# Kernel tuning notes

Hardware: AMD Instinct MI355X
Metric: run time of the kernel (lower is better)

The kernel has to match this reference:

```python
import jax, jax.numpy as jnp
import numpy as np

NEG = -1e9

def setup_inputs() -> dict:
    key = jax.random.key(0)
    k1, k2, k3, k4 = jax.random.split(key, 4)
    L, B, D = 4096, 4, 64
    query = jax.random.normal(k1, (L, B, D), dtype=jnp.float32)
    kkey = jax.random.normal(k2, (L, B, D), dtype=jnp.float32)
    value = jax.random.normal(k3, (L, B, D), dtype=jnp.float32)
    key_padding_mask = jax.random.randint(k4, (B, L), 0, 2).astype(jnp.bool_)
    return {"query": query, "key": kkey, "value": value, "key_padding_mask": key_padding_mask}

def reference(query, key, value, key_padding_mask):
    # [L, B, D] -> [B, L, D]
    scaling = float(query.shape[-1]) ** (-0.5)
    q = jnp.transpose(query, (1, 0, 2)) * scaling
    k = jnp.transpose(key, (1, 0, 2))
    v = jnp.transpose(value, (1, 0, 2))
    attn = jnp.einsum('bqd,bkd->bqk', q, k)  # [B, Lq, Lk]
    attn = jnp.where(key_padding_mask[:, None, :], NEG, attn)
    attn = jax.nn.softmax(attn, axis=-1)  # dropout p=0 -> identity
    out = jnp.einsum('bqk,bkd->bqd', attn, v)
    return jnp.transpose(out, (1, 0, 2)), attn
```

## Files before the change

kernel.cpp:

```cpp
#include <hip/hip_runtime.h>
#include <math.h>

#define L_ 4096
#define B_ 4
#define D_ 64
#define JS 8

typedef float f32x4 __attribute__((ext_vector_type(4)));
typedef int   i32x4 __attribute__((ext_vector_type(4)));
typedef short bf16x8 __attribute__((ext_vector_type(8)));
typedef unsigned short u16x8 __attribute__((ext_vector_type(8)));
typedef unsigned short u16x4 __attribute__((ext_vector_type(4)));

#define MFMA16(a, b, c) __builtin_amdgcn_mfma_f32_16x16x32_bf16(a, b, c, 0, 0, 0)

__device__ inline unsigned short f2bf(float x) {
    union { float f; unsigned int u; } v; v.f = x;
    unsigned int r = v.u + 0x7FFFu + ((v.u >> 16) & 1u);
    return (unsigned short)(r >> 16);
}
__device__ inline float bf2f(unsigned short h) {
    union { unsigned int u; float f; } v; v.u = ((unsigned int)h) << 16;
    return v.f;
}

__device__ inline void stage64(const unsigned short* __restrict__ g,
                               unsigned short* l, int tid) {
    const int w  = tid >> 6;
    const int ln = tid & 63;
#pragma unroll
    for (int r2 = 0; r2 < 2; ++r2) {
        const int base = r2 * 4096 + w * 1024;
        const int d = base + ln * 16;
        const int s = d ^ (((d >> 7) & 7) << 4);
        __builtin_amdgcn_global_load_lds(
            (const __attribute__((address_space(1))) void*)((const char*)g + s),
            (__attribute__((address_space(3))) void*)((char*)l + base),
            16, 0, 0);
    }
}

__device__ inline bf16x8 rdfrag(const unsigned short* l, int row, int colh) {
    int off = (row << 7) + (colh << 1);
    off ^= (row & 7) << 4;
    return *(const bf16x8*)((const char*)l + off);
}

__global__ void zero_out_kernel(float* __restrict__ out) {
    const int i = blockIdx.x * 256 + threadIdx.x;
    ((f32x4*)out)[i] = (f32x4){0.f, 0.f, 0.f, 0.f};
}

__device__ inline void convert16(const float* __restrict__ src,
                                 unsigned short* __restrict__ dhi,
                                 unsigned short* __restrict__ dlo) {
    f32x4 a[4];
#pragma unroll
    for (int i = 0; i < 4; ++i) a[i] = *(const f32x4*)(src + 4 * i);
    u16x8 h0, h1, lo0, lo1;
#pragma unroll
    for (int m = 0; m < 16; ++m) {
        float x = a[m >> 2][m & 3];
        unsigned short h = f2bf(x);
        unsigned short l = f2bf(x - bf2f(h));
        if (m < 8) { h0[m] = (short)h; lo0[m] = (short)l; }
        else       { h1[m - 8] = (short)h; lo1[m - 8] = (short)l; }
    }
    *(u16x8*)(dhi)     = h0;  *(u16x8*)(dhi + 8) = h1;
    *(u16x8*)(dlo)     = lo0; *(u16x8*)(dlo + 8) = lo1;
}

__global__ __launch_bounds__(256) void prep_kernel(
    const float* __restrict__ Q, const float* __restrict__ K, const float* __restrict__ V,
    unsigned short* __restrict__ Qhi, unsigned short* __restrict__ Qlo,
    unsigned short* __restrict__ Khi, unsigned short* __restrict__ Klo,
    unsigned short* __restrict__ Vthi, unsigned short* __restrict__ Vtlo) {
    __shared__ __align__(16) float vt[64][68];
    const int t  = threadIdx.x;
    const int b  = blockIdx.x >> 6;
    const int l0 = (blockIdx.x & 63) << 6;
    const int r  = t >> 2;
    const int d0 = (t & 3) << 4;

    const size_t src = (size_t)(l0 + r) * (B_ * D_) + (size_t)b * D_ + d0;
    const size_t dst = ((size_t)b * L_ + l0 + r) * D_ + d0;
    convert16(Q + src, Qhi + dst, Qlo + dst);
    convert16(K + src, Khi + dst, Klo + dst);

    const float* vsrc = V + src;
#pragma unroll
    for (int m = 0; m < 16; m += 4)
        *(f32x4*)&vt[r][d0 + m] = *(const f32x4*)&vsrc[m];
    __syncthreads();

    const int d  = t >> 2;
    const int lp = (t & 3) << 4;
    u16x8 h0, h1, lo0, lo1;
#pragma unroll
    for (int m = 0; m < 16; ++m) {
        float x = vt[lp + m][d];
        unsigned short h = f2bf(x);
        unsigned short l = f2bf(x - bf2f(h));
        if (m < 8) { h0[m] = (short)h; lo0[m] = (short)l; }
        else       { h1[m - 8] = (short)h; lo1[m - 8] = (short)l; }
    }
    unsigned short* oh = Vthi + ((size_t)b * D_ + d) * L_ + l0 + lp;
    unsigned short* ol = Vtlo + ((size_t)b * D_ + d) * L_ + l0 + lp;
    *(u16x8*)(oh) = h0;  *(u16x8*)(oh + 8) = h1;
    *(u16x8*)(ol) = lo0; *(u16x8*)(ol + 8) = lo1;
}

__global__ __launch_bounds__(256) void stats_kernel(
    const unsigned short* __restrict__ Qhi, const unsigned short* __restrict__ Qlo,
    const unsigned short* __restrict__ Khi, const unsigned short* __restrict__ Klo,
    const int* __restrict__ mask, float* __restrict__ lpart)
{
    __shared__ __align__(16) unsigned short kh[2][64 * 64];
    __shared__ __align__(16) unsigned short kl[2][64 * 64];

    const int tid = threadIdx.x;
    const int w = tid >> 6, lane = tid & 63;
    const int lr = lane & 15, lg = lane >> 4;
    const int b  = blockIdx.x >> 8;
    const int it = (blockIdx.x >> 3) & 31;
    const int jc = blockIdx.x & 7;
    const int irow = it * 128 + w * 32;
    const int j0c  = jc * (L_ / JS);

    bf16x8 qh0[2], qh1[2], ql0[2], ql1[2];
#pragma unroll
    for (int rs = 0; rs < 2; ++rs) {
        const size_t qoff = ((size_t)b * L_ + irow + rs * 16 + lr) * D_ + lg * 8;
        qh0[rs] = *(const bf16x8*)(Qhi + qoff);
        qh1[rs] = *(const bf16x8*)(Qhi + qoff + 32);
        ql0[rs] = *(const bf16x8*)(Qlo + qoff);
        ql1[rs] = *(const bf16x8*)(Qlo + qoff + 32);
    }

    float lsum[2] = {0.f, 0.f};
    int buf = 0;
    stage64(Khi + ((size_t)b * L_ + j0c) * D_, kh[0], tid);
    stage64(Klo + ((size_t)b * L_ + j0c) * D_, kl[0], tid);
    __syncthreads();

    for (int st = 0; st < (L_ / JS) / 64; ++st) {
        const int j0 = j0c + st * 64;
        if (st < (L_ / JS) / 64 - 1) {
            stage64(Khi + ((size_t)b * L_ + j0 + 64) * D_, kh[buf ^ 1], tid);
            stage64(Klo + ((size_t)b * L_ + j0 + 64) * D_, kl[buf ^ 1], tid);
        }
#pragma unroll
        for (int jj = 0; jj < 4; ++jj) {
            const bf16x8 a_h0 = rdfrag(kh[buf], jj * 16 + lr, lg * 8);
            const bf16x8 a_h1 = rdfrag(kh[buf], jj * 16 + lr, lg * 8 + 32);
            const bf16x8 a_l0 = rdfrag(kl[buf], jj * 16 + lr, lg * 8);
            const bf16x8 a_l1 = rdfrag(kl[buf], jj * 16 + lr, lg * 8 + 32);
            const i32x4 mv = *(const i32x4*)&mask[(size_t)b * L_ + j0 + jj * 16 + lg * 4];
            f32x4 bias;
#pragma unroll
            for (int r = 0; r < 4; ++r) bias[r] = mv[r] ? -1.0e9f : 0.0f;
#pragma unroll
            for (int rs = 0; rs < 2; ++rs) {
                f32x4 acc = {0.f, 0.f, 0.f, 0.f};
                acc = MFMA16(a_h0, qh0[rs], acc);
                acc = MFMA16(a_h1, qh1[rs], acc);
                acc = MFMA16(a_h0, ql0[rs], acc);
                acc = MFMA16(a_h1, ql1[rs], acc);
                acc = MFMA16(a_l0, qh0[rs], acc);
                acc = MFMA16(a_l1, qh1[rs], acc);
#pragma unroll
                for (int r = 0; r < 4; ++r)
                    lsum[rs] += __expf(fmaf(acc[r], 0.125f, bias[r]) - 32.0f);
            }
        }
        __syncthreads();
        buf ^= 1;
    }
#pragma unroll
    for (int rs = 0; rs < 2; ++rs) {
        float v = lsum[rs];
        v += __shfl_xor(v, 16, 64);
        v += __shfl_xor(v, 32, 64);
        if (lg == 0)
            lpart[((size_t)b * L_ + irow + rs * 16 + lr) * JS + jc] = v;
    }
}

__global__ __launch_bounds__(256) void pv_kernel(
    const unsigned short* __restrict__ Qhi, const unsigned short* __restrict__ Qlo,
    const unsigned short* __restrict__ Khi, const unsigned short* __restrict__ Klo,
    const unsigned short* __restrict__ Vthi, const unsigned short* __restrict__ Vtlo,
    const int* __restrict__ mask, const float* __restrict__ lpart,
    float* __restrict__ attn, float* __restrict__ out)
{
    __shared__ __align__(16) unsigned short kh[2][64 * 64];
    __shared__ __align__(16) unsigned short kl[2][64 * 64];
    __shared__ __align__(16) unsigned short phs[4][16][72];
    __shared__ __align__(16) unsigned short pls[4][16][72];

    const int tid = threadIdx.x;
    const int w = tid >> 6, lane = tid & 63;
    const int lr = lane & 15, lg = lane >> 4;
    const int b  = blockIdx.x >> 8;
    const int it = (blockIdx.x >> 3) & 31;
    const int jc = blockIdx.x & 7;
    const int irow = it * 128 + w * 32;
    const int j0c  = jc * (L_ / JS);
    const size_t ab = (size_t)b * L_ * L_;

    bf16x8 qh0[2], qh1[2], ql0[2], ql1[2];
    float invl[2];
#pragma unroll
    for (int rs = 0; rs < 2; ++rs) {
        const size_t row = (size_t)b * L_ + irow + rs * 16 + lr;
        const size_t qoff = row * D_ + lg * 8;
        qh0[rs] = *(const bf16x8*)(Qhi + qoff);
        qh1[rs] = *(const bf16x8*)(Qhi + qoff + 32);
        ql0[rs] = *(const bf16x8*)(Qlo + qoff);
        ql1[rs] = *(const bf16x8*)(Qlo + qoff + 32);
        const float* lp = lpart + row * JS;
        f32x4 s0 = *(const f32x4*)lp;
        f32x4 s1 = *(const f32x4*)(lp + 4);
        invl[rs] = 1.0f / (s0[0] + s0[1] + s0[2] + s0[3] + s1[0] + s1[1] + s1[2] + s1[3]);
    }

    f32x4 oacc[2][4];
#pragma unroll
    for (int rs = 0; rs < 2; ++rs)
#pragma unroll
        for (int dv = 0; dv < 4; ++dv) oacc[rs][dv] = (f32x4){0.f, 0.f, 0.f, 0.f};

    int buf = 0;
    stage64(Khi + ((size_t)b * L_ + j0c) * D_, kh[0], tid);
    stage64(Klo + ((size_t)b * L_ + j0c) * D_, kl[0], tid);
    __syncthreads();

    for (int st = 0; st < (L_ / JS) / 64; ++st) {
        const int j0 = j0c + st * 64;
        if (st < (L_ / JS) / 64 - 1) {
            stage64(Khi + ((size_t)b * L_ + j0 + 64) * D_, kh[buf ^ 1], tid);
            stage64(Klo + ((size_t)b * L_ + j0 + 64) * D_, kl[buf ^ 1], tid);
        }
#pragma unroll
        for (int rs = 0; rs < 2; ++rs) {
#pragma unroll
            for (int jj = 0; jj < 4; ++jj) {
                const bf16x8 a_h0 = rdfrag(kh[buf], jj * 16 + lr, lg * 8);
                const bf16x8 a_h1 = rdfrag(kh[buf], jj * 16 + lr, lg * 8 + 32);
                const bf16x8 a_l0 = rdfrag(kl[buf], jj * 16 + lr, lg * 8);
                const bf16x8 a_l1 = rdfrag(kl[buf], jj * 16 + lr, lg * 8 + 32);
                const i32x4 mv = *(const i32x4*)&mask[(size_t)b * L_ + j0 + jj * 16 + lg * 4];
                f32x4 acc = {0.f, 0.f, 0.f, 0.f};
                acc = MFMA16(a_h0, qh0[rs], acc);
                acc = MFMA16(a_h1, qh1[rs], acc);
                acc = MFMA16(a_h0, ql0[rs], acc);
                acc = MFMA16(a_h1, ql1[rs], acc);
                acc = MFMA16(a_l0, qh0[rs], acc);
                acc = MFMA16(a_l1, qh1[rs], acc);
                f32x4 p4;
                u16x4 hv, lv;
#pragma unroll
                for (int r = 0; r < 4; ++r) {
                    const float bias = mv[r] ? -1.0e9f : 0.0f;
                    const float p = __expf(fmaf(acc[r], 0.125f, bias) - 32.0f) * invl[rs];
                    p4[r] = p;
                    const unsigned short h = f2bf(p);
                    hv[r] = h;
                    lv[r] = f2bf(p - bf2f(h));
                }
                *(f32x4*)&attn[ab + (size_t)(irow + rs * 16 + lr) * L_ + j0 + jj * 16 + lg * 4] = p4;
                *(u16x4*)&phs[w][lr][jj * 16 + lg * 4] = hv;
                *(u16x4*)&pls[w][lr][jj * 16 + lg * 4] = lv;
            }
#pragma unroll
            for (int kk = 0; kk < 2; ++kk) {
                const bf16x8 ph = *(const bf16x8*)&phs[w][lr][kk * 32 + lg * 8];
                const bf16x8 pl = *(const bf16x8*)&pls[w][lr][kk * 32 + lg * 8];
#pragma unroll
                for (int dv = 0; dv < 4; ++dv) {
                    const size_t voff = ((size_t)b * D_ + dv * 16 + lr) * L_ + j0 + kk * 32 + lg * 8;
                    const bf16x8 vh = *(const bf16x8*)(Vthi + voff);
                    const bf16x8 vl = *(const bf16x8*)(Vtlo + voff);
                    oacc[rs][dv] = MFMA16(vh, ph, oacc[rs][dv]);
                    oacc[rs][dv] = MFMA16(vh, pl, oacc[rs][dv]);
                    oacc[rs][dv] = MFMA16(vl, ph, oacc[rs][dv]);
                }
            }
        }
        __syncthreads();
        buf ^= 1;
    }

#pragma unroll
    for (int rs = 0; rs < 2; ++rs)
#pragma unroll
        for (int dv = 0; dv < 4; ++dv) {
            const size_t obase = (size_t)(irow + rs * 16 + lr) * (B_ * D_) + b * D_ + dv * 16 + lg * 4;
#pragma unroll
            for (int r = 0; r < 4; ++r)
                atomicAdd(&out[obase + r], oacc[rs][dv][r]);
        }
}

extern "C" void kernel_launch(void* const* d_in, const int* in_sizes, int n_in,
                              void* d_out, int out_size, void* d_ws, size_t ws_size,
                              hipStream_t stream) {
    const float* Q   = (const float*)d_in[0];
    const float* K   = (const float*)d_in[1];
    const float* V   = (const float*)d_in[2];
    const int*  mask = (const int*)d_in[3];

    float* out  = (float*)d_out;
    float* attn = (float*)d_out + (size_t)L_ * B_ * D_;

    const size_t NE = (size_t)B_ * L_ * D_;
    unsigned short* Qhi  = (unsigned short*)d_ws;
    unsigned short* Qlo  = Qhi + NE;
    unsigned short* Khi  = Qhi + 2 * NE;
    unsigned short* Klo  = Qhi + 3 * NE;
    unsigned short* Vthi = Qhi + 4 * NE;
    unsigned short* Vtlo = Qhi + 5 * NE;
    float* lpart = (float*)((char*)d_ws + 6 * NE * sizeof(unsigned short));

    hipLaunchKernelGGL(zero_out_kernel, dim3((L_ * B_ * D_) / (256 * 4)), dim3(256), 0, stream, out);
    hipLaunchKernelGGL(prep_kernel, dim3(B_ * (L_ / 64)), dim3(256), 0, stream,
                       Q, K, V, Qhi, Qlo, Khi, Klo, Vthi, Vtlo);
    hipLaunchKernelGGL(stats_kernel, dim3(B_ * (L_ / 128) * JS), dim3(256), 0, stream,
                       Qhi, Qlo, Khi, Klo, mask, lpart);
    hipLaunchKernelGGL(pv_kernel, dim3(B_ * (L_ / 128) * JS), dim3(256), 0, stream,
                       Qhi, Qlo, Khi, Klo, Vthi, Vtlo, mask, lpart, attn, out);
}
```

Measured before the change: 579.4 us.

## Fuse stats and PV passes into one kernel, normalize attention afterwards

Removes the separate softmax-denominator kernel, which recomputed the full QK^T product. One kernel now computes the unnormalized exponentials once, writes them to attn, feeds them to the PV MFMAs, and emits partial row sums. New rescale and finalize kernels then divide attn and out by the summed denominator. The 1/sqrt(D) scale is folded into Q during prep, and the exponent no longer subtracts a fixed offset. The trade-offs are an extra full read and write of the large attn matrix, and the loss of K-tile double buffering in the fused loop.

```diff
diff --git a/kernel.cpp b/kernel.cpp
--- a/kernel.cpp
+++ b/kernel.cpp
@@ -51,7 +51,7 @@
     ((f32x4*)out)[i] = (f32x4){0.f, 0.f, 0.f, 0.f};
 }
 
-__device__ inline void convert16(const float* __restrict__ src,
+__device__ inline void convert16(const float* __restrict__ src, float scale,
                                  unsigned short* __restrict__ dhi,
                                  unsigned short* __restrict__ dlo) {
     f32x4 a[4];
@@ -60,7 +60,7 @@
     u16x8 h0, h1, lo0, lo1;
 #pragma unroll
     for (int m = 0; m < 16; ++m) {
-        float x = a[m >> 2][m & 3];
+        float x = a[m >> 2][m & 3] * scale;
         unsigned short h = f2bf(x);
         unsigned short l = f2bf(x - bf2f(h));
         if (m < 8) { h0[m] = (short)h; lo0[m] = (short)l; }
@@ -84,8 +84,8 @@
 
     const size_t src = (size_t)(l0 + r) * (B_ * D_) + (size_t)b * D_ + d0;
     const size_t dst = ((size_t)b * L_ + l0 + r) * D_ + d0;
-    convert16(Q + src, Qhi + dst, Qlo + dst);
-    convert16(K + src, Khi + dst, Klo + dst);
+    convert16(Q + src, 0.125f, Qhi + dst, Qlo + dst);
+    convert16(K + src, 1.0f,   Khi + dst, Klo + dst);
 
     const float* vsrc = V + src;
 #pragma unroll
@@ -110,91 +110,15 @@
     *(u16x8*)(ol) = lo0; *(u16x8*)(ol + 8) = lo1;
 }
 
-__global__ __launch_bounds__(256) void stats_kernel(
-    const unsigned short* __restrict__ Qhi, const unsigned short* __restrict__ Qlo,
-    const unsigned short* __restrict__ Khi, const unsigned short* __restrict__ Klo,
-    const int* __restrict__ mask, float* __restrict__ lpart)
-{
-    __shared__ __align__(16) unsigned short kh[2][64 * 64];
-    __shared__ __align__(16) unsigned short kl[2][64 * 64];
-
-    const int tid = threadIdx.x;
-    const int w = tid >> 6, lane = tid & 63;
-    const int lr = lane & 15, lg = lane >> 4;
-    const int b  = blockIdx.x >> 8;
-    const int it = (blockIdx.x >> 3) & 31;
-    const int jc = blockIdx.x & 7;
-    const int irow = it * 128 + w * 32;
-    const int j0c  = jc * (L_ / JS);
-
-    bf16x8 qh0[2], qh1[2], ql0[2], ql1[2];
-#pragma unroll
-    for (int rs = 0; rs < 2; ++rs) {
-        const size_t qoff = ((size_t)b * L_ + irow + rs * 16 + lr) * D_ + lg * 8;
-        qh0[rs] = *(const bf16x8*)(Qhi + qoff);
-        qh1[rs] = *(const bf16x8*)(Qhi + qoff + 32);
-        ql0[rs] = *(const bf16x8*)(Qlo + qoff);
-        ql1[rs] = *(const bf16x8*)(Qlo + qoff + 32);
-    }
-
-    float lsum[2] = {0.f, 0.f};
-    int buf = 0;
-    stage64(Khi + ((size_t)b * L_ + j0c) * D_, kh[0], tid);
-    stage64(Klo + ((size_t)b * L_ + j0c) * D_, kl[0], tid);
-    __syncthreads();
-
-    for (int st = 0; st < (L_ / JS) / 64; ++st) {
-        const int j0 = j0c + st * 64;
-        if (st < (L_ / JS) / 64 - 1) {
-            stage64(Khi + ((size_t)b * L_ + j0 + 64) * D_, kh[buf ^ 1], tid);
-            stage64(Klo + ((size_t)b * L_ + j0 + 64) * D_, kl[buf ^ 1], tid);
-        }
-#pragma unroll
-        for (int jj = 0; jj < 4; ++jj) {
-            const bf16x8 a_h0 = rdfrag(kh[buf], jj * 16 + lr, lg * 8);
-            const bf16x8 a_h1 = rdfrag(kh[buf], jj * 16 + lr, lg * 8 + 32);
-            const bf16x8 a_l0 = rdfrag(kl[buf], jj * 16 + lr, lg * 8);
-            const bf16x8 a_l1 = rdfrag(kl[buf], jj * 16 + lr, lg * 8 + 32);
-            const i32x4 mv = *(const i32x4*)&mask[(size_t)b * L_ + j0 + jj * 16 + lg * 4];
-            f32x4 bias;
-#pragma unroll
-            for (int r = 0; r < 4; ++r) bias[r] = mv[r] ? -1.0e9f : 0.0f;
-#pragma unroll
-            for (int rs = 0; rs < 2; ++rs) {
-                f32x4 acc = {0.f, 0.f, 0.f, 0.f};
-                acc = MFMA16(a_h0, qh0[rs], acc);
-                acc = MFMA16(a_h1, qh1[rs], acc);
-                acc = MFMA16(a_h0, ql0[rs], acc);
-                acc = MFMA16(a_h1, ql1[rs], acc);
-                acc = MFMA16(a_l0, qh0[rs], acc);
-                acc = MFMA16(a_l1, qh1[rs], acc);
-#pragma unroll
-                for (int r = 0; r < 4; ++r)
-                    lsum[rs] += __expf(fmaf(acc[r], 0.125f, bias[r]) - 32.0f);
-            }
-        }
-        __syncthreads();
-        buf ^= 1;
-    }
-#pragma unroll
-    for (int rs = 0; rs < 2; ++rs) {
-        float v = lsum[rs];
-        v += __shfl_xor(v, 16, 64);
-        v += __shfl_xor(v, 32, 64);
-        if (lg == 0)
-            lpart[((size_t)b * L_ + irow + rs * 16 + lr) * JS + jc] = v;
-    }
-}
-
-__global__ __launch_bounds__(256) void pv_kernel(
+__global__ __launch_bounds__(256) void fused_kernel(
     const unsigned short* __restrict__ Qhi, const unsigned short* __restrict__ Qlo,
     const unsigned short* __restrict__ Khi, const unsigned short* __restrict__ Klo,
     const unsigned short* __restrict__ Vthi, const unsigned short* __restrict__ Vtlo,
-    const int* __restrict__ mask, const float* __restrict__ lpart,
-    float* __restrict__ attn, float* __restrict__ out)
+    const int* __restrict__ mask, float* __restrict__ attn,
+    float* __restrict__ lpart, float* __restrict__ out)
 {
-    __shared__ __align__(16) unsigned short kh[2][64 * 64];
-    __shared__ __align__(16) unsigned short kl[2][64 * 64];
+    __shared__ __align__(16) unsigned short kh[64 * 64];
+    __shared__ __align__(16) unsigned short kl[64 * 64];
     __shared__ __align__(16) unsigned short phs[4][16][72];
     __shared__ __align__(16) unsigned short pls[4][16][72];
 
@@ -209,19 +133,13 @@
     const size_t ab = (size_t)b * L_ * L_;
 
     bf16x8 qh0[2], qh1[2], ql0[2], ql1[2];
-    float invl[2];
 #pragma unroll
     for (int rs = 0; rs < 2; ++rs) {
-        const size_t row = (size_t)b * L_ + irow + rs * 16 + lr;
-        const size_t qoff = row * D_ + lg * 8;
+        const size_t qoff = ((size_t)b * L_ + irow + rs * 16 + lr) * D_ + lg * 8;
         qh0[rs] = *(const bf16x8*)(Qhi + qoff);
         qh1[rs] = *(const bf16x8*)(Qhi + qoff + 32);
         ql0[rs] = *(const bf16x8*)(Qlo + qoff);
         ql1[rs] = *(const bf16x8*)(Qlo + qoff + 32);
-        const float* lp = lpart + row * JS;
-        f32x4 s0 = *(const f32x4*)lp;
-        f32x4 s1 = *(const f32x4*)(lp + 4);
-        invl[rs] = 1.0f / (s0[0] + s0[1] + s0[2] + s0[3] + s1[0] + s1[1] + s1[2] + s1[3]);
     }
 
     f32x4 oacc[2][4];
@@ -229,27 +147,29 @@
     for (int rs = 0; rs < 2; ++rs)
 #pragma unroll
         for (int dv = 0; dv < 4; ++dv) oacc[rs][dv] = (f32x4){0.f, 0.f, 0.f, 0.f};
-
-    int buf = 0;
-    stage64(Khi + ((size_t)b * L_ + j0c) * D_, kh[0], tid);
-    stage64(Klo + ((size_t)b * L_ + j0c) * D_, kl[0], tid);
-    __syncthreads();
+    float lsum[2] = {0.f, 0.f};
 
     for (int st = 0; st < (L_ / JS) / 64; ++st) {
         const int j0 = j0c + st * 64;
-        if (st < (L_ / JS) / 64 - 1) {
-            stage64(Khi + ((size_t)b * L_ + j0 + 64) * D_, kh[buf ^ 1], tid);
-            stage64(Klo + ((size_t)b * L_ + j0 + 64) * D_, kl[buf ^ 1], tid);
-        }
+        __syncthreads();
+        stage64(Khi + ((size_t)b * L_ + j0) * D_, kh, tid);
+        stage64(Klo + ((size_t)b * L_ + j0) * D_, kl, tid);
+        __syncthreads();
+
+        i32x4 mv[4];
+#pragma unroll
+        for (int jj = 0; jj < 4; ++jj)
+            mv[jj] = *(const i32x4*)&mask[(size_t)b * L_ + j0 + jj * 16 + lg * 4];
+
+        bf16x8 P[2][4];
 #pragma unroll
         for (int rs = 0; rs < 2; ++rs) {
 #pragma unroll
             for (int jj = 0; jj < 4; ++jj) {
-                const bf16x8 a_h0 = rdfrag(kh[buf], jj * 16 + lr, lg * 8);
-                const bf16x8 a_h1 = rdfrag(kh[buf], jj * 16 + lr, lg * 8 + 32);
-                const bf16x8 a_l0 = rdfrag(kl[buf], jj * 16 + lr, lg * 8);
-                const bf16x8 a_l1 = rdfrag(kl[buf], jj * 16 + lr, lg * 8 + 32);
-                const i32x4 mv = *(const i32x4*)&mask[(size_t)b * L_ + j0 + jj * 16 + lg * 4];
+                const bf16x8 a_h0 = rdfrag(kh, jj * 16 + lr, lg * 8);
+                const bf16x8 a_h1 = rdfrag(kh, jj * 16 + lr, lg * 8 + 32);
+                const bf16x8 a_l0 = rdfrag(kl, jj * 16 + lr, lg * 8);
+                const bf16x8 a_l1 = rdfrag(kl, jj * 16 + lr, lg * 8 + 32);
                 f32x4 acc = {0.f, 0.f, 0.f, 0.f};
                 acc = MFMA16(a_h0, qh0[rs], acc);
                 acc = MFMA16(a_h1, qh1[rs], acc);
@@ -257,42 +177,51 @@
                 acc = MFMA16(a_h1, ql1[rs], acc);
                 acc = MFMA16(a_l0, qh0[rs], acc);
                 acc = MFMA16(a_l1, qh1[rs], acc);
-                f32x4 p4;
+                f32x4 e4;
                 u16x4 hv, lv;
 #pragma unroll
                 for (int r = 0; r < 4; ++r) {
-                    const float bias = mv[r] ? -1.0e9f : 0.0f;
-                    const float p = __expf(fmaf(acc[r], 0.125f, bias) - 32.0f) * invl[rs];
-                    p4[r] = p;
-                    const unsigned short h = f2bf(p);
+                    const float s = mv[jj][r] ? -1.0e9f : acc[r];
+                    const float e = __expf(s);
+                    e4[r] = e;
+                    const unsigned short h = f2bf(e);
                     hv[r] = h;
-                    lv[r] = f2bf(p - bf2f(h));
+                    lv[r] = f2bf(e - bf2f(h));
                 }
-                *(f32x4*)&attn[ab + (size_t)(irow + rs * 16 + lr) * L_ + j0 + jj * 16 + lg * 4] = p4;
+                lsum[rs] += e4[0] + e4[1] + e4[2] + e4[3];
+                *(f32x4*)&attn[ab + (size_t)(irow + rs * 16 + lr) * L_ + j0 + jj * 16 + lg * 4] = e4;
                 *(u16x4*)&phs[w][lr][jj * 16 + lg * 4] = hv;
                 *(u16x4*)&pls[w][lr][jj * 16 + lg * 4] = lv;
             }
-#pragma unroll
-            for (int kk = 0; kk < 2; ++kk) {
-                const bf16x8 ph = *(const bf16x8*)&phs[w][lr][kk * 32 + lg * 8];
-                const bf16x8 pl = *(const bf16x8*)&pls[w][lr][kk * 32 + lg * 8];
-#pragma unroll
-                for (int dv = 0; dv < 4; ++dv) {
-                    const size_t voff = ((size_t)b * D_ + dv * 16 + lr) * L_ + j0 + kk * 32 + lg * 8;
-                    const bf16x8 vh = *(const bf16x8*)(Vthi + voff);
-                    const bf16x8 vl = *(const bf16x8*)(Vtlo + voff);
-                    oacc[rs][dv] = MFMA16(vh, ph, oacc[rs][dv]);
-                    oacc[rs][dv] = MFMA16(vh, pl, oacc[rs][dv]);
-                    oacc[rs][dv] = MFMA16(vl, ph, oacc[rs][dv]);
+            P[rs][0] = *(const bf16x8*)&phs[w][lr][lg * 8];
+            P[rs][1] = *(const bf16x8*)&pls[w][lr][lg * 8];
+            P[rs][2] = *(const bf16x8*)&phs[w][lr][32 + lg * 8];
+            P[rs][3] = *(const bf16x8*)&pls[w][lr][32 + lg * 8];
+        }
+#pragma unroll
+        for (int kk = 0; kk < 2; ++kk) {
+#pragma unroll
+            for (int dv = 0; dv < 4; ++dv) {
+                const size_t voff = ((size_t)b * D_ + dv * 16 + lr) * L_ + j0 + kk * 32 + lg * 8;
+                const bf16x8 vh = *(const bf16x8*)(Vthi + voff);
+                const bf16x8 vl = *(const bf16x8*)(Vtlo + voff);
+#pragma unroll
+                for (int rs = 0; rs < 2; ++rs) {
+                    oacc[rs][dv] = MFMA16(vh, P[rs][kk * 2], oacc[rs][dv]);
+                    oacc[rs][dv] = MFMA16(vh, P[rs][kk * 2 + 1], oacc[rs][dv]);
+                    oacc[rs][dv] = MFMA16(vl, P[rs][kk * 2], oacc[rs][dv]);
                 }
             }
         }
-        __syncthreads();
-        buf ^= 1;
-    }
-
-#pragma unroll
-    for (int rs = 0; rs < 2; ++rs)
+    }
+
+#pragma unroll
+    for (int rs = 0; rs < 2; ++rs) {
+        float v = lsum[rs];
+        v += __shfl_xor(v, 16, 64);
+        v += __shfl_xor(v, 32, 64);
+        if (lg == 0)
+            lpart[((size_t)b * L_ + irow + rs * 16 + lr) * JS + jc] = v;
 #pragma unroll
         for (int dv = 0; dv < 4; ++dv) {
             const size_t obase = (size_t)(irow + rs * 16 + lr) * (B_ * D_) + b * D_ + dv * 16 + lg * 4;
@@ -300,6 +229,43 @@
             for (int r = 0; r < 4; ++r)
                 atomicAdd(&out[obase + r], oacc[rs][dv][r]);
         }
+    }
+}
+
+__global__ __launch_bounds__(256) void rescale_kernel(
+    float* __restrict__ attn, const float* __restrict__ lpart)
+{
+    const int row = blockIdx.x;
+    const float* lp = lpart + (size_t)row * JS;
+    float l = 0.f;
+#pragma unroll
+    for (int k = 0; k < JS; ++k) l += lp[k];
+    const float invl = 1.0f / l;
+
+    float* base = attn + (size_t)row * L_;
+    const int t = threadIdx.x;
+#pragma unroll
+    for (int k = 0; k < 4; ++k) {
+        f32x4 v = *(f32x4*)&base[(k * 256 + t) * 4];
+        v[0] *= invl; v[1] *= invl; v[2] *= invl; v[3] *= invl;
+        *(f32x4*)&base[(k * 256 + t) * 4] = v;
+    }
+}
+
+__global__ __launch_bounds__(256) void finalize_kernel(
+    float* __restrict__ out, const float* __restrict__ lpart)
+{
+    const int idx = blockIdx.x * 256 + threadIdx.x;
+    const int lb  = idx >> 4;
+    const int l   = lb >> 2, b = lb & 3;
+    const float* lp = lpart + ((size_t)b * L_ + l) * JS;
+    float s = 0.f;
+#pragma unroll
+    for (int k = 0; k < JS; ++k) s += lp[k];
+    const float invl = 1.0f / s;
+    f32x4 v = ((f32x4*)out)[idx];
+    v[0] *= invl; v[1] *= invl; v[2] *= invl; v[3] *= invl;
+    ((f32x4*)out)[idx] = v;
 }
 
 extern "C" void kernel_launch(void* const* d_in, const int* in_sizes, int n_in,
@@ -325,8 +291,9 @@
     hipLaunchKernelGGL(zero_out_kernel, dim3((L_ * B_ * D_) / (256 * 4)), dim3(256), 0, stream, out);
     hipLaunchKernelGGL(prep_kernel, dim3(B_ * (L_ / 64)), dim3(256), 0, stream,
                        Q, K, V, Qhi, Qlo, Khi, Klo, Vthi, Vtlo);
-    hipLaunchKernelGGL(stats_kernel, dim3(B_ * (L_ / 128) * JS), dim3(256), 0, stream,
-                       Qhi, Qlo, Khi, Klo, mask, lpart);
-    hipLaunchKernelGGL(pv_kernel, dim3(B_ * (L_ / 128) * JS), dim3(256), 0, stream,
-                       Qhi, Qlo, Khi, Klo, Vthi, Vtlo, mask, lpart, attn, out);
-}
+    hipLaunchKernelGGL(fused_kernel, dim3(B_ * (L_ / 128) * JS), dim3(256), 0, stream,
+                       Qhi, Qlo, Khi, Klo, Vthi, Vtlo, mask, attn, lpart, out);
+    hipLaunchKernelGGL(rescale_kernel, dim3(B_ * L_), dim3(256), 0, stream, attn, lpart);
+    hipLaunchKernelGGL(finalize_kernel, dim3((L_ * B_ * D_) / (256 * 4)), dim3(256), 0, stream,
+                       out, lpart);
+}
```

Result: faster. 525.6 us (-9.3%).

## Fold softmax scale into Q prep and reuse V fragments across row sets

Applied to the files above, without the earlier changes.

The 1/sqrt(D) scale moves into the Q bf16 split in the prep kernel, and the constant -32 shift is dropped from both exp passes. This removes an fma and a subtract per score element. In the PV kernel, V fragments and mask words are now loaded once per 64-key step and shared by both 16-row sets, where before they were reloaded inside the row-set loop. The P-times-V MFMAs are regrouped after both P tiles are built. The K tile is now single-buffered with two barriers per step, which gives up the prefetch overlap and raises register pressure. Dropping the shift also gives up its overflow headroom in exp.

```diff
diff --git a/kernel.cpp b/kernel.cpp
--- a/kernel.cpp
+++ b/kernel.cpp
@@ -5,6 +5,7 @@
 #define B_ 4
 #define D_ 64
 #define JS 8
+#define NS ((L_ / JS) / 64)
 
 typedef float f32x4 __attribute__((ext_vector_type(4)));
 typedef int   i32x4 __attribute__((ext_vector_type(4)));
@@ -51,7 +52,7 @@
     ((f32x4*)out)[i] = (f32x4){0.f, 0.f, 0.f, 0.f};
 }
 
-__device__ inline void convert16(const float* __restrict__ src,
+__device__ inline void convert16(const float* __restrict__ src, float scale,
                                  unsigned short* __restrict__ dhi,
                                  unsigned short* __restrict__ dlo) {
     f32x4 a[4];
@@ -60,7 +61,7 @@
     u16x8 h0, h1, lo0, lo1;
 #pragma unroll
     for (int m = 0; m < 16; ++m) {
-        float x = a[m >> 2][m & 3];
+        float x = a[m >> 2][m & 3] * scale;
         unsigned short h = f2bf(x);
         unsigned short l = f2bf(x - bf2f(h));
         if (m < 8) { h0[m] = (short)h; lo0[m] = (short)l; }
@@ -84,8 +85,8 @@
 
     const size_t src = (size_t)(l0 + r) * (B_ * D_) + (size_t)b * D_ + d0;
     const size_t dst = ((size_t)b * L_ + l0 + r) * D_ + d0;
-    convert16(Q + src, Qhi + dst, Qlo + dst);
-    convert16(K + src, Khi + dst, Klo + dst);
+    convert16(Q + src, 0.125f, Qhi + dst, Qlo + dst);
+    convert16(K + src, 1.0f,   Khi + dst, Klo + dst);
 
     const float* vsrc = V + src;
 #pragma unroll
@@ -143,9 +144,9 @@
     stage64(Klo + ((size_t)b * L_ + j0c) * D_, kl[0], tid);
     __syncthreads();
 
-    for (int st = 0; st < (L_ / JS) / 64; ++st) {
+    for (int st = 0; st < NS; ++st) {
         const int j0 = j0c + st * 64;
-        if (st < (L_ / JS) / 64 - 1) {
+        if (st < NS - 1) {
             stage64(Khi + ((size_t)b * L_ + j0 + 64) * D_, kh[buf ^ 1], tid);
             stage64(Klo + ((size_t)b * L_ + j0 + 64) * D_, kl[buf ^ 1], tid);
         }
@@ -156,9 +157,6 @@
             const bf16x8 a_l0 = rdfrag(kl[buf], jj * 16 + lr, lg * 8);
             const bf16x8 a_l1 = rdfrag(kl[buf], jj * 16 + lr, lg * 8 + 32);
             const i32x4 mv = *(const i32x4*)&mask[(size_t)b * L_ + j0 + jj * 16 + lg * 4];
-            f32x4 bias;
-#pragma unroll
-            for (int r = 0; r < 4; ++r) bias[r] = mv[r] ? -1.0e9f : 0.0f;
 #pragma unroll
             for (int rs = 0; rs < 2; ++rs) {
                 f32x4 acc = {0.f, 0.f, 0.f, 0.f};
@@ -170,12 +168,13 @@
                 acc = MFMA16(a_l1, qh1[rs], acc);
 #pragma unroll
                 for (int r = 0; r < 4; ++r)
-                    lsum[rs] += __expf(fmaf(acc[r], 0.125f, bias[r]) - 32.0f);
+                    lsum[rs] += __expf(mv[r] ? -1.0e9f : acc[r]);
             }
         }
         __syncthreads();
         buf ^= 1;
     }
+
 #pragma unroll
     for (int rs = 0; rs < 2; ++rs) {
         float v = lsum[rs];
@@ -193,8 +192,8 @@
     const int* __restrict__ mask, const float* __restrict__ lpart,
     float* __restrict__ attn, float* __restrict__ out)
 {
-    __shared__ __align__(16) unsigned short kh[2][64 * 64];
-    __shared__ __align__(16) unsigned short kl[2][64 * 64];
+    __shared__ __align__(16) unsigned short kh[64 * 64];
+    __shared__ __align__(16) unsigned short kl[64 * 64];
     __shared__ __align__(16) unsigned short phs[4][16][72];
     __shared__ __align__(16) unsigned short pls[4][16][72];
 
@@ -230,26 +229,35 @@
 #pragma unroll
         for (int dv = 0; dv < 4; ++dv) oacc[rs][dv] = (f32x4){0.f, 0.f, 0.f, 0.f};
 
-    int buf = 0;
-    stage64(Khi + ((size_t)b * L_ + j0c) * D_, kh[0], tid);
-    stage64(Klo + ((size_t)b * L_ + j0c) * D_, kl[0], tid);
-    __syncthreads();
-
-    for (int st = 0; st < (L_ / JS) / 64; ++st) {
+    for (int st = 0; st < NS; ++st) {
         const int j0 = j0c + st * 64;
-        if (st < (L_ / JS) / 64 - 1) {
-            stage64(Khi + ((size_t)b * L_ + j0 + 64) * D_, kh[buf ^ 1], tid);
-            stage64(Klo + ((size_t)b * L_ + j0 + 64) * D_, kl[buf ^ 1], tid);
-        }
+        __syncthreads();
+        stage64(Khi + ((size_t)b * L_ + j0) * D_, kh, tid);
+        stage64(Klo + ((size_t)b * L_ + j0) * D_, kl, tid);
+        __syncthreads();
+
+        bf16x8 v0h[4], v0l[4];
+#pragma unroll
+        for (int dv = 0; dv < 4; ++dv) {
+            const size_t voff = ((size_t)b * D_ + dv * 16 + lr) * L_ + j0 + lg * 8;
+            v0h[dv] = *(const bf16x8*)(Vthi + voff);
+            v0l[dv] = *(const bf16x8*)(Vtlo + voff);
+        }
+
+        i32x4 mv[4];
+#pragma unroll
+        for (int jj = 0; jj < 4; ++jj)
+            mv[jj] = *(const i32x4*)&mask[(size_t)b * L_ + j0 + jj * 16 + lg * 4];
+
+        bf16x8 P[2][4];
 #pragma unroll
         for (int rs = 0; rs < 2; ++rs) {
 #pragma unroll
             for (int jj = 0; jj < 4; ++jj) {
-                const bf16x8 a_h0 = rdfrag(kh[buf], jj * 16 + lr, lg * 8);
-                const bf16x8 a_h1 = rdfrag(kh[buf], jj * 16 + lr, lg * 8 + 32);
-                const bf16x8 a_l0 = rdfrag(kl[buf], jj * 16 + lr, lg * 8);
-                const bf16x8 a_l1 = rdfrag(kl[buf], jj * 16 + lr, lg * 8 + 32);
-                const i32x4 mv = *(const i32x4*)&mask[(size_t)b * L_ + j0 + jj * 16 + lg * 4];
+                const bf16x8 a_h0 = rdfrag(kh, jj * 16 + lr, lg * 8);
+                const bf16x8 a_h1 = rdfrag(kh, jj * 16 + lr, lg * 8 + 32);
+                const bf16x8 a_l0 = rdfrag(kl, jj * 16 + lr, lg * 8);
+                const bf16x8 a_l1 = rdfrag(kl, jj * 16 + lr, lg * 8 + 32);
                 f32x4 acc = {0.f, 0.f, 0.f, 0.f};
                 acc = MFMA16(a_h0, qh0[rs], acc);
                 acc = MFMA16(a_h1, qh1[rs], acc);
@@ -261,8 +269,8 @@
                 u16x4 hv, lv;
 #pragma unroll
                 for (int r = 0; r < 4; ++r) {
-                    const float bias = mv[r] ? -1.0e9f : 0.0f;
-                    const float p = __expf(fmaf(acc[r], 0.125f, bias) - 32.0f) * invl[rs];
+                    const float e = __expf(mv[jj][r] ? -1.0e9f : acc[r]);
+                    const float p = e * invl[rs];
                     p4[r] = p;
                     const unsigned short h = f2bf(p);
                     hv[r] = h;
@@ -272,23 +280,36 @@
                 *(u16x4*)&phs[w][lr][jj * 16 + lg * 4] = hv;
                 *(u16x4*)&pls[w][lr][jj * 16 + lg * 4] = lv;
             }
-#pragma unroll
-            for (int kk = 0; kk < 2; ++kk) {
-                const bf16x8 ph = *(const bf16x8*)&phs[w][lr][kk * 32 + lg * 8];
-                const bf16x8 pl = *(const bf16x8*)&pls[w][lr][kk * 32 + lg * 8];
-#pragma unroll
-                for (int dv = 0; dv < 4; ++dv) {
-                    const size_t voff = ((size_t)b * D_ + dv * 16 + lr) * L_ + j0 + kk * 32 + lg * 8;
-                    const bf16x8 vh = *(const bf16x8*)(Vthi + voff);
-                    const bf16x8 vl = *(const bf16x8*)(Vtlo + voff);
-                    oacc[rs][dv] = MFMA16(vh, ph, oacc[rs][dv]);
-                    oacc[rs][dv] = MFMA16(vh, pl, oacc[rs][dv]);
-                    oacc[rs][dv] = MFMA16(vl, ph, oacc[rs][dv]);
-                }
+            P[rs][0] = *(const bf16x8*)&phs[w][lr][lg * 8];
+            P[rs][1] = *(const bf16x8*)&pls[w][lr][lg * 8];
+            P[rs][2] = *(const bf16x8*)&phs[w][lr][32 + lg * 8];
+            P[rs][3] = *(const bf16x8*)&pls[w][lr][32 + lg * 8];
+        }
+
+        bf16x8 v1h[4], v1l[4];
+#pragma unroll
+        for (int dv = 0; dv < 4; ++dv) {
+            const size_t voff = ((size_t)b * D_ + dv * 16 + lr) * L_ + j0 + 32 + lg * 8;
+            v1h[dv] = *(const bf16x8*)(Vthi + voff);
+            v1l[dv] = *(const bf16x8*)(Vtlo + voff);
+        }
+
+#pragma unroll
+        for (int dv = 0; dv < 4; ++dv)
+#pragma unroll
+            for (int rs = 0; rs < 2; ++rs) {
+                oacc[rs][dv] = MFMA16(v0h[dv], P[rs][0], oacc[rs][dv]);
+                oacc[rs][dv] = MFMA16(v0h[dv], P[rs][1], oacc[rs][dv]);
+                oacc[rs][dv] = MFMA16(v0l[dv], P[rs][0], oacc[rs][dv]);
             }
-        }
-        __syncthreads();
-        buf ^= 1;
+#pragma unroll
+        for (int dv = 0; dv < 4; ++dv)
+#pragma unroll
+            for (int rs = 0; rs < 2; ++rs) {
+                oacc[rs][dv] = MFMA16(v1h[dv], P[rs][2], oacc[rs][dv]);
+                oacc[rs][dv] = MFMA16(v1h[dv], P[rs][3], oacc[rs][dv]);
+                oacc[rs][dv] = MFMA16(v1l[dv], P[rs][2], oacc[rs][dv]);
+            }
     }
 
 #pragma unroll
```

Result: faster. 469.1 us (-19.0%).
